# Optimization experiments

Hardware: AMD Instinct MI355X
Metric: run time of the kernel (lower is better)

## Reference

```python
import jax, jax.numpy as jnp
import numpy as np


def setup_inputs() -> dict:
    key = jax.random.key(0)
    k1, k2 = jax.random.split(key)
    x = jax.random.normal(k1, (32, 64, 64, 64), dtype=jnp.float32)  # [B, C, H, W]
    limit = 3 ** 0.5
    embeddings = jax.random.uniform(k2, (64, 512), dtype=jnp.float32,
                                    minval=-limit, maxval=limit)  # [D, K]
    return {"x": x, "embeddings": embeddings}


def reference(x, embeddings):
    B, D, H, W = x.shape
    # NCHW -> NHWC -> [N, D]
    flat_x = jnp.transpose(x, (0, 2, 3, 1)).reshape(-1, D)
    distances = (
        jnp.sum(flat_x ** 2, axis=1, keepdims=True)
        - 2.0 * flat_x @ embeddings
        + jnp.sum(embeddings ** 2, axis=0, keepdims=True)
    )
    encoding_indices = jnp.argmin(distances, axis=1)  # [N]
    # gather codebook rows: embeddings.T is [K, D]
    quantized = embeddings.T[encoding_indices].reshape(B, H, W, D)
    quantized = jnp.transpose(quantized, (0, 3, 1, 2))  # back to NCHW
    commitment_loss = jnp.mean((x - jax.lax.stop_gradient(quantized)) ** 2)
    # straight-through estimator
    quantized_ste = x + jax.lax.stop_gradient(quantized - x)
    return quantized_ste, commitment_loss, encoding_indices.reshape(B, -1)
```

## Files before the change

kernel.cpp:

```cpp
#include <hip/hip_runtime.h>

#define D      64
#define K      512
#define Q_OFF  0
#define L_OFF  8388608
#define I_OFF  8388609

#define WS_ET    0
#define WS_EN    32768
#define WS_ENH   33280
#define WS_PART  33792

#define B_LO_OFF 4096

typedef __attribute__((ext_vector_type(8))) short short8;
typedef __attribute__((ext_vector_type(4))) float f32x4;

static __device__ __forceinline__ unsigned short f2bf(float f) {
    unsigned u = __float_as_uint(f);
    u += 0x7fffu + ((u >> 16) & 1u);
    return (unsigned short)(u >> 16);
}
static __device__ __forceinline__ float bf2f(unsigned short h) {
    return __uint_as_float(((unsigned)h) << 16);
}

__global__ __launch_bounds__(256) void vq_prep(const float* __restrict__ E,
                                               float* __restrict__ ws,
                                               float* __restrict__ out) {
    int g = blockIdx.x * 256 + threadIdx.x;
    int t = g >> 6, lane = g & 63;
    int col = lane & 15, kg = lane >> 4;
    int code = t * 16 + col;
    short8* bhp = (short8*)out;
    short8* blp = (short8*)out + B_LO_OFF;
#pragma unroll
    for (int s = 0; s < 2; ++s) {
        short8 h, l;
#pragma unroll
        for (int j = 0; j < 8; ++j) {
            int k = s * 32 + kg * 8 + j;
            float v = -E[k * K + code];
            unsigned short hb = f2bf(v);
            h[j] = (short)hb;
            l[j] = (short)f2bf(v - bf2f(hb));
        }
        bhp[(t * 2 + s) * 64 + lane] = h;
        blp[(t * 2 + s) * 64 + lane] = l;
    }
    if (g < K) {
        float nsq = 0.f;
#pragma unroll 8
        for (int d = 0; d < D; ++d) {
            float v = E[d * K + g];
            ws[WS_ET + g * D + d] = v;
            nsq = fmaf(v, v, nsq);
        }
        ws[WS_EN + g]  = nsq;
        ws[WS_ENH + g] = 0.5f * nsq;
    }
}

__global__ __launch_bounds__(256, 2) void vq_dist(const float* __restrict__ x,
                                                  const float* __restrict__ ws,
                                                  float* __restrict__ out) {
    const int tid = threadIdx.x, w = tid >> 6, lane = tid & 63;
    const int col = lane & 15, rowg = lane >> 4;
    const int pixw = blockIdx.x * 128 + w * 32;

    short8 ah[2][2], al[2][2];
#pragma unroll
    for (int mt = 0; mt < 2; ++mt) {
        int pix = pixw + mt * 16 + col;
        const float* xp = x + ((size_t)(pix >> 12) << 18) + (pix & 4095);
#pragma unroll
        for (int s = 0; s < 2; ++s) {
            short8 h, l;
#pragma unroll
            for (int j = 0; j < 8; ++j) {
                float v = xp[(size_t)(s * 32 + rowg * 8 + j) << 12];
                unsigned short hb = f2bf(v);
                h[j] = (short)hb;
                l[j] = (short)f2bf(v - bf2f(hb));
            }
            ah[mt][s] = h; al[mt][s] = l;
        }
    }

    const short8* bhp = (const short8*)out;
    const short8* blp = (const short8*)out + B_LO_OFF;
    const float*  enh = ws + WS_ENH;

    float b1[2][4], b2[2][4]; int i1[2][4], i2[2][4];
#pragma unroll
    for (int mt = 0; mt < 2; ++mt)
#pragma unroll
        for (int r = 0; r < 4; ++r) {
            b1[mt][r] = 3.4e38f; b2[mt][r] = 3.4e38f;
            i1[mt][r] = 0;       i2[mt][r] = 0;
        }

    short8 cbh0[2], cbh1[2], cbl0[2], cbl1[2]; float cenh[2];
    cbh0[0] = bhp[lane];      cbh1[0] = bhp[64 + lane];
    cbl0[0] = blp[lane];      cbl1[0] = blp[64 + lane];
    cenh[0] = enh[col];

#pragma unroll 2
    for (int t = 0; t < 32; ++t) {
        const int cur = t & 1, nxt = cur ^ 1;
        if (t + 1 < 32) {
            int o = (t + 1) * 128;
            cbh0[nxt] = bhp[o + lane];      cbh1[nxt] = bhp[o + 64 + lane];
            cbl0[nxt] = blp[o + lane];      cbl1[nxt] = blp[o + 64 + lane];
            cenh[nxt] = enh[(t + 1) * 16 + col];
        }
        const float ev = cenh[cur];
        const int codev = t * 16 + col;
#pragma unroll
        for (int mt = 0; mt < 2; ++mt) {
            f32x4 acc = { ev, ev, ev, ev };
            acc = __builtin_amdgcn_mfma_f32_16x16x32_bf16(ah[mt][0], cbh0[cur], acc, 0, 0, 0);
            acc = __builtin_amdgcn_mfma_f32_16x16x32_bf16(al[mt][0], cbh0[cur], acc, 0, 0, 0);
            acc = __builtin_amdgcn_mfma_f32_16x16x32_bf16(ah[mt][0], cbl0[cur], acc, 0, 0, 0);
            acc = __builtin_amdgcn_mfma_f32_16x16x32_bf16(ah[mt][1], cbh1[cur], acc, 0, 0, 0);
            acc = __builtin_amdgcn_mfma_f32_16x16x32_bf16(al[mt][1], cbh1[cur], acc, 0, 0, 0);
            acc = __builtin_amdgcn_mfma_f32_16x16x32_bf16(ah[mt][1], cbl1[cur], acc, 0, 0, 0);
#pragma unroll
            for (int r = 0; r < 4; ++r) {
                float v = acc[r];
                bool lt  = v < b1[mt][r];
                float lv = lt ? b1[mt][r] : v;
                int   li = lt ? i1[mt][r] : codev;
                b1[mt][r] = lt ? v : b1[mt][r];
                i1[mt][r] = lt ? codev : i1[mt][r];
                bool lt2 = lv < b2[mt][r];
                b2[mt][r] = lt2 ? lv : b2[mt][r];
                i2[mt][r] = lt2 ? li : i2[mt][r];
            }
        }
    }

    unsigned* outu = (unsigned*)out;
#pragma unroll
    for (int mt = 0; mt < 2; ++mt)
#pragma unroll
        for (int r = 0; r < 4; ++r) {
            float vb1 = b1[mt][r], vb2 = b2[mt][r];
            int   vi1 = i1[mt][r], vi2 = i2[mt][r];
#pragma unroll
            for (int m = 1; m < 16; m <<= 1) {
                float ob1 = __shfl_xor(vb1, m, 16);
                float ob2 = __shfl_xor(vb2, m, 16);
                int   oi1 = __shfl_xor(vi1, m, 16);
                int   oi2 = __shfl_xor(vi2, m, 16);
                bool lt   = ob1 < vb1;
                float nb1 = lt ? ob1 : vb1;  int ni1 = lt ? oi1 : vi1;
                float l1v = lt ? vb1 : ob1;  int l1i = lt ? vi1 : oi1;
                float cb2 = lt ? ob2 : vb2;  int ci2 = lt ? oi2 : vi2;
                bool lt2  = cb2 < l1v;
                vb2 = lt2 ? cb2 : l1v;  vi2 = lt2 ? ci2 : l1i;
                vb1 = nb1;              vi1 = ni1;
            }
            if (col == r) {
                int p = pixw + mt * 16 + rowg * 4 + r;
                outu[I_OFF + p] = (unsigned)vi1 | ((unsigned)vi2 << 16);
            }
        }
}

__device__ __forceinline__ float dotrow(const float* __restrict__ er,
                                        const float* __restrict__ xv) {
    const float4* e4 = (const float4*)er;
    float a0 = 0.f, a1 = 0.f, a2 = 0.f, a3 = 0.f;
#pragma unroll
    for (int q = 0; q < 16; ++q) {
        float4 e = e4[q];
        a0 = fmaf(xv[4*q+0], e.x, a0);
        a1 = fmaf(xv[4*q+1], e.y, a1);
        a2 = fmaf(xv[4*q+2], e.z, a2);
        a3 = fmaf(xv[4*q+3], e.w, a3);
    }
    return (a0 + a1) + (a2 + a3);
}

__global__ __launch_bounds__(256) void vq_out(const float* __restrict__ x,
                                              const float* __restrict__ ws,
                                              float* __restrict__ out,
                                              float* __restrict__ partial) {
    const float* ET = ws + WS_ET;
    const float* EN = ws + WS_EN;
    int n  = blockIdx.x * 256 + threadIdx.x;
    int b  = n >> 12;
    int hw = n & 4095;

    const float* xp = x + ((size_t)b << 18) + hw;
    float xv[D];
#pragma unroll
    for (int d = 0; d < D; ++d) xv[d] = xp[(size_t)d << 12];

    unsigned packed = ((const unsigned*)out)[I_OFF + n];
    int c1 = (int)(packed & 0xffffu), c2 = (int)(packed >> 16);

    float d1 = fmaf(-2.f, dotrow(ET + (c1 << 6), xv), EN[c1]);
    float d2 = fmaf(-2.f, dotrow(ET + (c2 << 6), xv), EN[c2]);
    bool sw = (d2 < d1) || (d2 == d1 && c2 < c1);
    int bestk = sw ? c2 : c1;

    out[I_OFF + n] = (float)bestk;

    const float* qv = ET + (bestk << 6);
    float* op = out + Q_OFF + ((size_t)b << 18) + hw;
    float lsum = 0.f;
#pragma unroll
    for (int d = 0; d < D; ++d) {
        float qd = qv[d];
        op[(size_t)d << 12] = qd;
        float diff = xv[d] - qd;
        lsum = fmaf(diff, diff, lsum);
    }

#pragma unroll
    for (int off = 32; off > 0; off >>= 1)
        lsum += __shfl_down(lsum, off, 64);
    __shared__ float wsum[4];
    if ((threadIdx.x & 63) == 0) wsum[threadIdx.x >> 6] = lsum;
    __syncthreads();
    if (threadIdx.x == 0)
        partial[blockIdx.x] = (wsum[0] + wsum[1]) + (wsum[2] + wsum[3]);
}

__global__ __launch_bounds__(256) void vq_final(const float* __restrict__ partial,
                                                float* __restrict__ out) {
    int t = threadIdx.x;
    float s = partial[t] + partial[t + 256];
#pragma unroll
    for (int off = 32; off > 0; off >>= 1)
        s += __shfl_down(s, off, 64);
    __shared__ float wsum[4];
    if ((t & 63) == 0) wsum[t >> 6] = s;
    __syncthreads();
    if (t == 0)
        out[L_OFF] = ((wsum[0] + wsum[1]) + (wsum[2] + wsum[3])) * (1.f / 8388608.f);
}

extern "C" void kernel_launch(void* const* d_in, const int* in_sizes, int n_in,
                              void* d_out, int out_size, void* d_ws, size_t ws_size,
                              hipStream_t stream) {
    const float* x = (const float*)d_in[0];
    const float* E = (const float*)d_in[1];
    float* out = (float*)d_out;
    float* ws  = (float*)d_ws;

    hipLaunchKernelGGL(vq_prep,  dim3(8),    dim3(256), 0, stream, E, ws, out);
    hipLaunchKernelGGL(vq_dist,  dim3(1024), dim3(256), 0, stream, x, ws, out);
    hipLaunchKernelGGL(vq_out,   dim3(512),  dim3(256), 0, stream, x, ws, out, ws + WS_PART);
    hipLaunchKernelGGL(vq_final, dim3(1),    dim3(256), 0, stream, ws + WS_PART, out);
}
```

Before: 71.16 us.

## Pack quantized distance and code index into one key for integer top-2

Replaces the float value/index top-2 tracking with a single 32-bit key: the distance is scaled and biased into a fixed-point integer, shifted left by 9 and ORed with the code index, so the selection becomes plain unsigned min/max and the cross-lane reduction shuffles two values instead of four. The codebook prefetch is also deepened to two iterations ahead and the two M-tiles' MFMA chains are interleaved. The quantization loses distance precision (about 2^-14 resolution, with a limited range) and can change tie-breaking among near-equal candidates. A later exact rescoring step over the top-2 candidates presumably guards correctness.

```diff
diff --git a/kernel.cpp b/kernel.cpp
--- a/kernel.cpp
+++ b/kernel.cpp
@@ -12,6 +12,9 @@
 #define WS_PART  33792
 
 #define B_LO_OFF 4096
+
+#define SEL_SCALE 16384.0f
+#define SEL_BIAS  (160.0f * 16384.0f)
 
 typedef __attribute__((ext_vector_type(8))) short short8;
 typedef __attribute__((ext_vector_type(4))) float f32x4;
@@ -91,52 +94,58 @@
     const short8* blp = (const short8*)out + B_LO_OFF;
     const float*  enh = ws + WS_ENH;
 
-    float b1[2][4], b2[2][4]; int i1[2][4], i2[2][4];
+    unsigned m1[2][4], m2[2][4];
 #pragma unroll
     for (int mt = 0; mt < 2; ++mt)
 #pragma unroll
-        for (int r = 0; r < 4; ++r) {
-            b1[mt][r] = 3.4e38f; b2[mt][r] = 3.4e38f;
-            i1[mt][r] = 0;       i2[mt][r] = 0;
-        }
-
-    short8 cbh0[2], cbh1[2], cbl0[2], cbl1[2]; float cenh[2];
-    cbh0[0] = bhp[lane];      cbh1[0] = bhp[64 + lane];
-    cbl0[0] = blp[lane];      cbl1[0] = blp[64 + lane];
-    cenh[0] = enh[col];
+        for (int r = 0; r < 4; ++r) { m1[mt][r] = 0xFFFFFFFFu; m2[mt][r] = 0xFFFFFFFFu; }
+
+    short8 pbh0[2], pbh1[2], pbl0[2], pbl1[2]; float pev[2];
+    pbh0[0] = bhp[lane];        pbh1[0] = bhp[64 + lane];
+    pbl0[0] = blp[lane];        pbl1[0] = blp[64 + lane];
+    pev[0]  = enh[col];
+    pbh0[1] = bhp[128 + lane];  pbh1[1] = bhp[192 + lane];
+    pbl0[1] = blp[128 + lane];  pbl1[1] = blp[192 + lane];
+    pev[1]  = enh[16 + col];
 
 #pragma unroll 2
     for (int t = 0; t < 32; ++t) {
-        const int cur = t & 1, nxt = cur ^ 1;
-        if (t + 1 < 32) {
-            int o = (t + 1) * 128;
-            cbh0[nxt] = bhp[o + lane];      cbh1[nxt] = bhp[o + 64 + lane];
-            cbl0[nxt] = blp[o + lane];      cbl1[nxt] = blp[o + 64 + lane];
-            cenh[nxt] = enh[(t + 1) * 16 + col];
-        }
-        const float ev = cenh[cur];
-        const int codev = t * 16 + col;
-#pragma unroll
-        for (int mt = 0; mt < 2; ++mt) {
-            f32x4 acc = { ev, ev, ev, ev };
-            acc = __builtin_amdgcn_mfma_f32_16x16x32_bf16(ah[mt][0], cbh0[cur], acc, 0, 0, 0);
-            acc = __builtin_amdgcn_mfma_f32_16x16x32_bf16(al[mt][0], cbh0[cur], acc, 0, 0, 0);
-            acc = __builtin_amdgcn_mfma_f32_16x16x32_bf16(ah[mt][0], cbl0[cur], acc, 0, 0, 0);
-            acc = __builtin_amdgcn_mfma_f32_16x16x32_bf16(ah[mt][1], cbh1[cur], acc, 0, 0, 0);
-            acc = __builtin_amdgcn_mfma_f32_16x16x32_bf16(al[mt][1], cbh1[cur], acc, 0, 0, 0);
-            acc = __builtin_amdgcn_mfma_f32_16x16x32_bf16(ah[mt][1], cbl1[cur], acc, 0, 0, 0);
-#pragma unroll
-            for (int r = 0; r < 4; ++r) {
-                float v = acc[r];
-                bool lt  = v < b1[mt][r];
-                float lv = lt ? b1[mt][r] : v;
-                int   li = lt ? i1[mt][r] : codev;
-                b1[mt][r] = lt ? v : b1[mt][r];
-                i1[mt][r] = lt ? codev : i1[mt][r];
-                bool lt2 = lv < b2[mt][r];
-                b2[mt][r] = lt2 ? lv : b2[mt][r];
-                i2[mt][r] = lt2 ? li : i2[mt][r];
-            }
+        const int cur = t & 1;
+        const float ev = pev[cur];
+        const unsigned codev = (unsigned)(t * 16 + col);
+
+        f32x4 acc0 = { ev, ev, ev, ev };
+        f32x4 acc1 = { ev, ev, ev, ev };
+        acc0 = __builtin_amdgcn_mfma_f32_16x16x32_bf16(ah[0][0], pbh0[cur], acc0, 0, 0, 0);
+        acc0 = __builtin_amdgcn_mfma_f32_16x16x32_bf16(al[0][0], pbh0[cur], acc0, 0, 0, 0);
+        acc0 = __builtin_amdgcn_mfma_f32_16x16x32_bf16(ah[0][0], pbl0[cur], acc0, 0, 0, 0);
+        acc0 = __builtin_amdgcn_mfma_f32_16x16x32_bf16(ah[0][1], pbh1[cur], acc0, 0, 0, 0);
+        acc0 = __builtin_amdgcn_mfma_f32_16x16x32_bf16(al[0][1], pbh1[cur], acc0, 0, 0, 0);
+        acc0 = __builtin_amdgcn_mfma_f32_16x16x32_bf16(ah[0][1], pbl1[cur], acc0, 0, 0, 0);
+        acc1 = __builtin_amdgcn_mfma_f32_16x16x32_bf16(ah[1][0], pbh0[cur], acc1, 0, 0, 0);
+        acc1 = __builtin_amdgcn_mfma_f32_16x16x32_bf16(al[1][0], pbh0[cur], acc1, 0, 0, 0);
+        acc1 = __builtin_amdgcn_mfma_f32_16x16x32_bf16(ah[1][0], pbl0[cur], acc1, 0, 0, 0);
+        acc1 = __builtin_amdgcn_mfma_f32_16x16x32_bf16(ah[1][1], pbh1[cur], acc1, 0, 0, 0);
+        acc1 = __builtin_amdgcn_mfma_f32_16x16x32_bf16(al[1][1], pbh1[cur], acc1, 0, 0, 0);
+        acc1 = __builtin_amdgcn_mfma_f32_16x16x32_bf16(ah[1][1], pbl1[cur], acc1, 0, 0, 0);
+
+        if (t + 2 < 32) {
+            int o = (t + 2) * 128;
+            pbh0[cur] = bhp[o + lane];      pbh1[cur] = bhp[o + 64 + lane];
+            pbl0[cur] = blp[o + lane];      pbl1[cur] = blp[o + 64 + lane];
+            pev[cur]  = enh[(t + 2) * 16 + col];
+        }
+
+#pragma unroll
+        for (int r = 0; r < 4; ++r) {
+            unsigned u0 = (unsigned)fmaf(acc0[r], SEL_SCALE, SEL_BIAS);
+            unsigned p0 = (u0 << 9) + codev;
+            m2[0][r] = min(m2[0][r], max(m1[0][r], p0));
+            m1[0][r] = min(m1[0][r], p0);
+            unsigned u1 = (unsigned)fmaf(acc1[r], SEL_SCALE, SEL_BIAS);
+            unsigned p1 = (u1 << 9) + codev;
+            m2[1][r] = min(m2[1][r], max(m1[1][r], p1));
+            m1[1][r] = min(m1[1][r], p1);
         }
     }
 
@@ -145,25 +154,18 @@
     for (int mt = 0; mt < 2; ++mt)
 #pragma unroll
         for (int r = 0; r < 4; ++r) {
-            float vb1 = b1[mt][r], vb2 = b2[mt][r];
-            int   vi1 = i1[mt][r], vi2 = i2[mt][r];
+            unsigned v1 = m1[mt][r], v2 = m2[mt][r];
 #pragma unroll
             for (int m = 1; m < 16; m <<= 1) {
-                float ob1 = __shfl_xor(vb1, m, 16);
-                float ob2 = __shfl_xor(vb2, m, 16);
-                int   oi1 = __shfl_xor(vi1, m, 16);
-                int   oi2 = __shfl_xor(vi2, m, 16);
-                bool lt   = ob1 < vb1;
-                float nb1 = lt ? ob1 : vb1;  int ni1 = lt ? oi1 : vi1;
-                float l1v = lt ? vb1 : ob1;  int l1i = lt ? vi1 : oi1;
-                float cb2 = lt ? ob2 : vb2;  int ci2 = lt ? oi2 : vi2;
-                bool lt2  = cb2 < l1v;
-                vb2 = lt2 ? cb2 : l1v;  vi2 = lt2 ? ci2 : l1i;
-                vb1 = nb1;              vi1 = ni1;
+                unsigned o1 = (unsigned)__shfl_xor((int)v1, m, 16);
+                unsigned o2 = (unsigned)__shfl_xor((int)v2, m, 16);
+                v2 = min(max(v1, o1), min(v2, o2));
+                v1 = min(v1, o1);
             }
             if (col == r) {
                 int p = pixw + mt * 16 + rowg * 4 + r;
-                outu[I_OFF + p] = (unsigned)vi1 | ((unsigned)vi2 << 16);
+                unsigned c1 = v1 & 511u, c2 = v2 & 511u;
+                outu[I_OFF + p] = c1 | (c2 << 16);
             }
         }
 }
```

Result: faster. 65.82 us (-7.5%).
